# Optimization experiments

Hardware: AMD Instinct MI355X
Metric: run time of the kernel (lower is better)

The kernel has to match this reference:

```python
import jax, jax.numpy as jnp
import numpy as np

E, C, K, S = 8, 128, 512, 512  # embedding_dim, channels, kernel_size, stride
NEG_SLOPE = 0.01  # torch F.leaky_relu default


def setup_inputs() -> dict:
    key = jax.random.key(0)
    ks = jax.random.split(key, 11)
    B, T = 4, 1_000_000
    sc = 0.05
    return {
        "x": jax.random.normal(ks[0], (B, T, E), jnp.float32),
        # ctx_conv: Conv1d(E, 2C, K, stride=S) -> weight (2C, E, K), bias (2C,)
        "ctx_conv_w": jax.random.normal(ks[1], (2 * C, E, K), jnp.float32) * sc,
        "ctx_conv_b": jax.random.normal(ks[2], (2 * C,), jnp.float32) * sc,
        # ctx_share: Conv1d(C, C, 1) -> (C, C) pointwise
        "ctx_share_w": jax.random.normal(ks[3], (C, C), jnp.float32) * sc,
        "ctx_share_b": jax.random.normal(ks[4], (C,), jnp.float32) * sc,
        "main_conv_w": jax.random.normal(ks[5], (2 * C, E, K), jnp.float32) * sc,
        "main_conv_b": jax.random.normal(ks[6], (2 * C,), jnp.float32) * sc,
        "main_share_w": jax.random.normal(ks[7], (C, C), jnp.float32) * sc,
        "main_share_b": jax.random.normal(ks[8], (C,), jnp.float32) * sc,
        # gct_proj: Linear(C, C) -> weight (C, C) (y = g @ W.T + b)
        "gct_proj_w": jax.random.normal(ks[9], (C, C), jnp.float32) * sc,
        "gct_proj_b": jax.random.normal(ks[10], (C,), jnp.float32) * sc,
    }


def _leaky(x):
    return jnp.where(x >= 0, x, NEG_SLOPE * x)


def _glu(x):  # GLU over channel dim 1
    a, b = jnp.split(x, 2, axis=1)
    return a * jax.nn.sigmoid(b)


def _conv(z, w, b):
    # z: (B, Cin, T), w: (Cout, Cin, K) -> (B, Cout, T_out), stride S, VALID
    y = jax.lax.conv_general_dilated(z, w, (S,), 'VALID',
                                     dimension_numbers=('NCH', 'OIH', 'NCH'))
    return y + b[None, :, None]


def _branch_act(z, wc, bc, ws, bs):
    # glu(conv(z)) -> leaky_relu(1x1 share conv)
    h = _glu(_conv(z, wc, bc))                                   # (B, C, T_out)
    h = _leaky(jnp.einsum('oc,bct->bot', ws, h) + bs[None, :, None])
    return h


def reference(x, ctx_conv_w, ctx_conv_b, ctx_share_w, ctx_share_b,
              main_conv_w, main_conv_b, main_share_w, main_share_b,
              gct_proj_w, gct_proj_b):
    z = jnp.transpose(x, (0, 2, 1))  # (B, E, T)
    # Context branch: global max over time of ctx activations (GCG context).
    g = _branch_act(z, ctx_conv_w, ctx_conv_b, ctx_share_w, ctx_share_b)
    gct = jnp.max(g, axis=-1)  # (B, C)
    # Main branch with global channel gating.
    h = _branch_act(z, main_conv_w, main_conv_b, main_share_w, main_share_b)  # (B, C, T_out)
    q = jnp.tanh(gct @ gct_proj_w.T + gct_proj_b)                # (B, C)
    gate = jax.nn.sigmoid(jnp.einsum('bct,bc->bt', h, q))        # (B, T_out)
    out = jnp.max(h * gate[:, None, :], axis=-1)                 # (B, C)
    return out
```

## Files before the change

kernel.cpp:

```cpp
#include <hip/hip_runtime.h>
#include <hip/hip_bf16.h>
#include <cmath>

#define B_    4
#define T_    1000000
#define E_    8
#define C_    128
#define NCH   512
#define KK    4096
#define TOUT  1953
#define TP    1956
#define TPAD  2048
#define NT2   31

typedef __attribute__((ext_vector_type(8))) short bf16x8;
typedef __attribute__((ext_vector_type(4))) float f32x4;

__device__ __forceinline__ float sigmoidf_(float v) { return 1.f / (1.f + __expf(-v)); }

__device__ __forceinline__ void gload_lds16(const __hip_bfloat16* g, __hip_bfloat16* l) {
  __builtin_amdgcn_global_load_lds(
      (const __attribute__((address_space(1))) void*)(const void*)g,
      (__attribute__((address_space(3))) void*)(void*)l, 16, 0, 0);
}

__global__ __launch_bounds__(256) void prep_inputs(
    const float* __restrict__ x,
    const float* __restrict__ wc, const float* __restrict__ bc,
    const float* __restrict__ wm, const float* __restrict__ bm,
    __hip_bfloat16* __restrict__ xb2, __hip_bfloat16* __restrict__ Wn2,
    float* __restrict__ bias_t) {
  __shared__ float row[KK];
  const int bid = blockIdx.x;
  if (bid < NCH) {
    const int n = bid, br = n >> 8, o = n & 255;
    const float* wsrc = (br ? wm : wc) + (size_t)o * KK;
    for (int i = threadIdx.x; i < KK; i += 256) row[i] = wsrc[i];
    __syncthreads();
    const int nt = n >> 4, nr = n & 15;
    for (int k = threadIdx.x; k < KK; k += 256) {
      int kpos = k >> 3, e = k & 7;
      size_t addr = (((size_t)nt * 128 + (k >> 5)) * 64
                     + (size_t)((k >> 3) & 3) * 16 + nr) * 8 + (k & 7);
      Wn2[addr] = __float2bfloat16(row[e * 512 + kpos]);
    }
    if (threadIdx.x == 0) bias_t[n] = (br ? bm : bc)[o];
  } else {
    size_t gid = (size_t)(bid - NCH) * 256 + threadIdx.x;
    size_t idx8 = gid * 8;
    size_t b = idx8 >> 23, rem = idx8 & ((1ull << 23) - 1);
    int lane = (int)((rem >> 3) & 63);
    int kc   = (int)((rem >> 9) & 127);
    int tt   = (int)(rem >> 16);
    int t = tt * 16 + (lane & 15);
    int k = kc * 32 + (lane >> 4) * 8;
    union { __hip_bfloat16 h[8]; uint4 u; } o;
    if (t < TOUT) {
      const float* src = x + b * 8000000ull + (size_t)t * KK + k;
      float4 f0 = *(const float4*)(src);
      float4 f1 = *(const float4*)(src + 4);
      o.h[0] = __float2bfloat16(f0.x); o.h[1] = __float2bfloat16(f0.y);
      o.h[2] = __float2bfloat16(f0.z); o.h[3] = __float2bfloat16(f0.w);
      o.h[4] = __float2bfloat16(f1.x); o.h[5] = __float2bfloat16(f1.y);
      o.h[6] = __float2bfloat16(f1.z); o.h[7] = __float2bfloat16(f1.w);
    } else {
      o.u = make_uint4(0, 0, 0, 0);
    }
    *(uint4*)(xb2 + idx8) = o.u;
  }
}

__global__ __launch_bounds__(512, 2) void mfma_gemm(
    const __hip_bfloat16* __restrict__ xb2, const __hip_bfloat16* __restrict__ Wn2,
    float* __restrict__ u2) {
  __shared__ __hip_bfloat16 lds[2][16384];

  const int tid  = threadIdx.x;
  const int lane = tid & 63, wave = tid >> 6;
  const int wt = wave & 3, wn = wave >> 2;

  const int L   = blockIdx.x;
  const int xcd = L & 7;
  const int r   = L >> 3;
  const int nb  = r & 3;
  const int sh  = r >> 2;
  const int s   = sh * 8 + xcd;
  const int tblk = s & 15, b = s >> 4;
  const int t0 = tblk * 128, n0 = nb * 128;

  const size_t FR = 512;

  const __hip_bfloat16* gsrc[4];
  int cslot[4];
#pragma unroll
  for (int s2 = 0; s2 < 4; ++s2) {
    int c = wave * 4 + s2;
    cslot[c & 3] = c;
    if (c < 16) {
      gsrc[s2] = xb2 + ((size_t)(b * 128 + tblk * 8 + (c >> 1)) * 128 + (c & 1)) * FR
                 + (size_t)lane * 8;
    } else {
      gsrc[s2] = Wn2 + ((size_t)(nb * 8 + ((c - 16) >> 1)) * 128 + (c & 1)) * FR
                 + (size_t)lane * 8;
    }
  }

  f32x4 acc[2][4];
#pragma unroll
  for (int i = 0; i < 2; ++i)
#pragma unroll
    for (int j = 0; j < 4; ++j) acc[i][j] = (f32x4)(0.0f);

  auto STAGE = [&](int buf, int step) {
#pragma unroll
    for (int s2 = 0; s2 < 4; ++s2) {
      gload_lds16(gsrc[s2] + (size_t)step * 1024, &lds[buf][(size_t)cslot[s2] * FR]);
    }
  };

  auto COMPUTE = [&](int buf) {
    bf16x8 aF[2][2], bF[4][2];
#pragma unroll
    for (int i = 0; i < 2; ++i)
#pragma unroll
      for (int c = 0; c < 2; ++c)
        aF[i][c] = *(const bf16x8*)(&lds[buf][(size_t)((wt * 2 + i) * 2 + c) * FR
                                              + (size_t)lane * 8]);
#pragma unroll
    for (int j = 0; j < 4; ++j)
#pragma unroll
      for (int c = 0; c < 2; ++c)
        bF[j][c] = *(const bf16x8*)(&lds[buf][(size_t)(16 + (wn * 4 + j) * 2 + c) * FR
                                              + (size_t)lane * 8]);
#pragma unroll
    for (int c = 0; c < 2; ++c)
#pragma unroll
      for (int i = 0; i < 2; ++i)
#pragma unroll
        for (int j = 0; j < 4; ++j)
          acc[i][j] = __builtin_amdgcn_mfma_f32_16x16x32_bf16(aF[i][c], bF[j][c],
                                                              acc[i][j], 0, 0, 0);
  };

  STAGE(0, 0);
  __syncthreads();

  int cur = 0;
#pragma unroll 1
  for (int step = 0; step < 64; ++step) {
    if (step + 1 < 64) STAGE(cur ^ 1, step + 1);
    COMPUTE(cur);
    __syncthreads();
    cur ^= 1;
  }

  const int crow = (lane >> 4) * 4;
  const int ccol = lane & 15;
#pragma unroll
  for (int j = 0; j < 4; ++j) {
    int n = n0 + wn * 64 + j * 16 + ccol;
    float* urow = u2 + ((size_t)n * B_ + b) * TP;
#pragma unroll
    for (int i = 0; i < 2; ++i) {
      int t = t0 + wt * 32 + i * 16 + crow;
      if (t < TOUT) *(f32x4*)(urow + t) = acc[i][j];
    }
  }
}

__global__ __launch_bounds__(256) void share_act(
    const float* __restrict__ u2, const float* __restrict__ bias_t,
    const float* __restrict__ wsc, const float* __restrict__ bsc,
    const float* __restrict__ wsm, const float* __restrict__ bsm,
    float* __restrict__ hmain, float* __restrict__ gct_part) {
  __shared__ float Wl[128 * 132];
  __shared__ float ul[128 * 68];
  const int tid  = threadIdx.x;
  const int tile = blockIdx.x;
  const int b    = blockIdx.y;
  const int br   = blockIdx.z;
  const int t0   = tile * 64;
  const float* ws = br ? wsm : wsc;
  const float* bs = br ? bsm : bsc;

  for (int g = tid; g < 16384; g += 256) {
    int co = g >> 7, cp = g & 127;
    Wl[cp * 132 + co] = ws[g];
  }
  const size_t base_v = ((size_t)(br * 256) * B_ + b) * TP;
  const size_t base_g = ((size_t)(br * 256 + 128) * B_ + b) * TP;
  for (int g = tid; g < 8192; g += 256) {
    int cp = g >> 6, t = g & 63;
    float v = 0.f;
    if (t0 + t < TOUT) {
      float va = u2[base_v + (size_t)cp * B_ * TP + t0 + t] + bias_t[br * 256 + cp];
      float vg = u2[base_g + (size_t)cp * B_ * TP + t0 + t] + bias_t[br * 256 + 128 + cp];
      v = va * sigmoidf_(vg);
    }
    ul[cp * 68 + t] = v;
  }
  __syncthreads();

  const int ty = tid >> 4, tx = tid & 15;
  float acc[8][4];
#pragma unroll
  for (int i = 0; i < 8; ++i)
#pragma unroll
    for (int j = 0; j < 4; ++j) acc[i][j] = 0.f;

  for (int cp = 0; cp < 128; ++cp) {
    float4 a0 = *(const float4*)&Wl[cp*132 + ty*4];
    float4 a1 = *(const float4*)&Wl[cp*132 + 64 + ty*4];
    float4 b4 = *(const float4*)&ul[cp*68 + tx*4];
    float av[8] = {a0.x,a0.y,a0.z,a0.w,a1.x,a1.y,a1.z,a1.w};
    float bv[4] = {b4.x,b4.y,b4.z,b4.w};
#pragma unroll
    for (int i = 0; i < 8; ++i)
#pragma unroll
      for (int j = 0; j < 4; ++j) acc[i][j] = fmaf(av[i], bv[j], acc[i][j]);
  }

  float mloc[8];
#pragma unroll
  for (int i = 0; i < 8; ++i) mloc[i] = -INFINITY;
#pragma unroll
  for (int i = 0; i < 8; ++i) {
    int c = (i < 4) ? (ty*4 + i) : (64 + ty*4 + (i - 4));
    float bias = bs[c];
#pragma unroll
    for (int j = 0; j < 4; ++j) {
      int t = t0 + tx*4 + j;
      if (t >= TOUT) continue;
      float v = acc[i][j] + bias;
      v = (v >= 0.f) ? v : 0.01f * v;
      if (br == 1) {
        hmain[((size_t)b * 128 + c) * TOUT + t] = v;
      } else {
        mloc[i] = fmaxf(mloc[i], v);
      }
    }
  }
  if (br == 0) {
    __syncthreads();
    float* red = ul;
#pragma unroll
    for (int i = 0; i < 8; ++i) {
      int c = (i < 4) ? (ty*4 + i) : (64 + ty*4 + (i - 4));
      red[c * 16 + tx] = mloc[i];
    }
    __syncthreads();
    if (tid < 128) {
      float m = -INFINITY;
#pragma unroll
      for (int k = 0; k < 16; ++k) m = fmaxf(m, red[tid * 16 + k]);
      gct_part[((size_t)b * 128 + tid) * NT2 + tile] = m;
    }
  }
}

__global__ void gct_q(const float* __restrict__ gct_part, const float* __restrict__ wp,
                      const float* __restrict__ bp, float* __restrict__ q) {
  int b = blockIdx.x, tid = threadIdx.x;
  __shared__ float g[128];
  float m = -INFINITY;
  for (int tl = 0; tl < NT2; ++tl) m = fmaxf(m, gct_part[((size_t)b * 128 + tid) * NT2 + tl]);
  g[tid] = m;
  __syncthreads();
  float s = bp[tid];
  for (int c = 0; c < 128; ++c) s = fmaf(g[c], wp[tid * 128 + c], s);
  q[b * 128 + tid] = tanhf(s);
}

__global__ __launch_bounds__(256) void gate_max(
    const float* __restrict__ hmain, const float* __restrict__ q,
    float* __restrict__ out_part) {
  __shared__ float hl[128 * 68];
  __shared__ float ql[128];
  __shared__ float red[256];
  __shared__ float gl[64];
  int tid = threadIdx.x, tile = blockIdx.x, b = blockIdx.y;
  int t0 = tile * 64;
  for (int g = tid; g < 8192; g += 256) {
    int c = g >> 6, t = g & 63;
    hl[c * 68 + t] = (t0 + t < TOUT) ? hmain[((size_t)b * 128 + c) * TOUT + t0 + t] : 0.f;
  }
  if (tid < 128) ql[tid] = q[b * 128 + tid];
  __syncthreads();
  {
    int t = tid & 63, cy = tid >> 6;
    float s = 0.f;
#pragma unroll
    for (int cc = 0; cc < 32; ++cc) s = fmaf(hl[(cy * 32 + cc) * 68 + t], ql[cy * 32 + cc], s);
    red[cy * 64 + t] = s;
  }
  __syncthreads();
  if (tid < 64) {
    float s = red[tid] + red[64 + tid] + red[128 + tid] + red[192 + tid];
    gl[tid] = sigmoidf_(s);
  }
  __syncthreads();
  {
    int c = tid >> 1, th = tid & 1;
    float m = -INFINITY;
#pragma unroll
    for (int tt = 0; tt < 32; ++tt) {
      int t = th * 32 + tt;
      if (t0 + t < TOUT) m = fmaxf(m, hl[c * 68 + t] * gl[t]);
    }
    red[c * 2 + th] = m;
  }
  __syncthreads();
  if (tid < 128) out_part[((size_t)b * 128 + tid) * NT2 + tile] = fmaxf(red[tid * 2], red[tid * 2 + 1]);
}

__global__ void final_max(const float* __restrict__ out_part, float* __restrict__ out) {
  int idx = blockIdx.x * 256 + threadIdx.x;
  if (idx < 512) {
    float m = -INFINITY;
    for (int tl = 0; tl < NT2; ++tl) m = fmaxf(m, out_part[(size_t)idx * NT2 + tl]);
    out[idx] = m;
  }
}

extern "C" void kernel_launch(void* const* d_in, const int* in_sizes, int n_in,
                              void* d_out, int out_size, void* d_ws, size_t ws_size,
                              hipStream_t stream) {
  const float* x      = (const float*)d_in[0];
  const float* ctx_w  = (const float*)d_in[1];
  const float* ctx_b  = (const float*)d_in[2];
  const float* ctx_sw = (const float*)d_in[3];
  const float* ctx_sb = (const float*)d_in[4];
  const float* main_w = (const float*)d_in[5];
  const float* main_b = (const float*)d_in[6];
  const float* main_sw= (const float*)d_in[7];
  const float* main_sb= (const float*)d_in[8];
  const float* gp_w   = (const float*)d_in[9];
  const float* gp_b   = (const float*)d_in[10];

  char* w = (char*)d_ws;
  __hip_bfloat16* xb2 = (__hip_bfloat16*)(w);
  __hip_bfloat16* Wn2 = (__hip_bfloat16*)(w + 67108864);
  float* bias_t  = (float*)(w + 71303168);
  float* u2      = (float*)(w + 71305216);
  float* hmain   = (float*)(w + 87328768);
  float* gct_part= (float*)(w + 91328512);
  float* q       = (float*)(w + 91392000);
  float* out_part= (float*)(w + 91394048);

  prep_inputs<<<NCH + 16384, 256, 0, stream>>>(x, ctx_w, ctx_b, main_w, main_b,
                                               xb2, Wn2, bias_t);
  mfma_gemm<<<256, 512, 0, stream>>>(xb2, Wn2, u2);
  share_act<<<dim3(NT2, B_, 2), 256, 0, stream>>>(u2, bias_t, ctx_sw, ctx_sb,
                                                  main_sw, main_sb, hmain, gct_part);
  gct_q<<<B_, 128, 0, stream>>>(gct_part, gp_w, gp_b, q);
  gate_max<<<dim3(NT2, B_), 256, 0, stream>>>(hmain, q, out_part);
  final_max<<<2, 256, 0, stream>>>(out_part, (float*)d_out);
}
```

Measured before the change: 309.4 us.

## Fuse x fp32-to-bf16 conversion into GEMM A-tile loading

Drops the separate pass that converts x to a bf16 tiled buffer. The GEMM now loads fp32 x directly into registers, converts it to bf16, and writes it to LDS, software-pipelined against the MFMA compute of the current buffer, while B still uses direct global-to-LDS loads. This avoids writing and rereading a 64MB intermediate and shrinks the workspace. In exchange, register pressure rises and the A path now goes through VGPRs, with possibly less-coalesced strided fp32 reads.

Measured after the change: 351.4 us. 13.6% more time.

```diff
diff --git a/kernel.cpp b/kernel.cpp
--- a/kernel.cpp
+++ b/kernel.cpp
@@ -10,7 +10,6 @@
 #define KK    4096
 #define TOUT  1953
 #define TP    1956
-#define TPAD  2048
 #define NT2   31
 
 typedef __attribute__((ext_vector_type(8))) short bf16x8;
@@ -25,55 +24,29 @@
 }
 
 __global__ __launch_bounds__(256) void prep_inputs(
-    const float* __restrict__ x,
     const float* __restrict__ wc, const float* __restrict__ bc,
     const float* __restrict__ wm, const float* __restrict__ bm,
-    __hip_bfloat16* __restrict__ xb2, __hip_bfloat16* __restrict__ Wn2,
-    float* __restrict__ bias_t) {
+    __hip_bfloat16* __restrict__ Wn2, float* __restrict__ bias_t) {
   __shared__ float row[KK];
-  const int bid = blockIdx.x;
-  if (bid < NCH) {
-    const int n = bid, br = n >> 8, o = n & 255;
-    const float* wsrc = (br ? wm : wc) + (size_t)o * KK;
-    for (int i = threadIdx.x; i < KK; i += 256) row[i] = wsrc[i];
-    __syncthreads();
-    const int nt = n >> 4, nr = n & 15;
-    for (int k = threadIdx.x; k < KK; k += 256) {
-      int kpos = k >> 3, e = k & 7;
-      size_t addr = (((size_t)nt * 128 + (k >> 5)) * 64
-                     + (size_t)((k >> 3) & 3) * 16 + nr) * 8 + (k & 7);
-      Wn2[addr] = __float2bfloat16(row[e * 512 + kpos]);
-    }
-    if (threadIdx.x == 0) bias_t[n] = (br ? bm : bc)[o];
-  } else {
-    size_t gid = (size_t)(bid - NCH) * 256 + threadIdx.x;
-    size_t idx8 = gid * 8;
-    size_t b = idx8 >> 23, rem = idx8 & ((1ull << 23) - 1);
-    int lane = (int)((rem >> 3) & 63);
-    int kc   = (int)((rem >> 9) & 127);
-    int tt   = (int)(rem >> 16);
-    int t = tt * 16 + (lane & 15);
-    int k = kc * 32 + (lane >> 4) * 8;
-    union { __hip_bfloat16 h[8]; uint4 u; } o;
-    if (t < TOUT) {
-      const float* src = x + b * 8000000ull + (size_t)t * KK + k;
-      float4 f0 = *(const float4*)(src);
-      float4 f1 = *(const float4*)(src + 4);
-      o.h[0] = __float2bfloat16(f0.x); o.h[1] = __float2bfloat16(f0.y);
-      o.h[2] = __float2bfloat16(f0.z); o.h[3] = __float2bfloat16(f0.w);
-      o.h[4] = __float2bfloat16(f1.x); o.h[5] = __float2bfloat16(f1.y);
-      o.h[6] = __float2bfloat16(f1.z); o.h[7] = __float2bfloat16(f1.w);
-    } else {
-      o.u = make_uint4(0, 0, 0, 0);
-    }
-    *(uint4*)(xb2 + idx8) = o.u;
-  }
+  const int n = blockIdx.x, br = n >> 8, o = n & 255;
+  const float* wsrc = (br ? wm : wc) + (size_t)o * KK;
+  for (int i = threadIdx.x; i < KK; i += 256) row[i] = wsrc[i];
+  __syncthreads();
+  const int nt = n >> 4, nr = n & 15;
+  for (int k = threadIdx.x; k < KK; k += 256) {
+    int kpos = k >> 3, e = k & 7;
+    size_t addr = (((size_t)nt * 128 + (k >> 5)) * 64
+                   + (size_t)((k >> 3) & 3) * 16 + nr) * 8 + (k & 7);
+    Wn2[addr] = __float2bfloat16(row[e * 512 + kpos]);
+  }
+  if (threadIdx.x == 0) bias_t[n] = (br ? bm : bc)[o];
 }
 
 __global__ __launch_bounds__(512, 2) void mfma_gemm(
-    const __hip_bfloat16* __restrict__ xb2, const __hip_bfloat16* __restrict__ Wn2,
+    const float* __restrict__ x, const __hip_bfloat16* __restrict__ Wn2,
     float* __restrict__ u2) {
-  __shared__ __hip_bfloat16 lds[2][16384];
+  __shared__ __hip_bfloat16 As[2][8192];
+  __shared__ __hip_bfloat16 Bs[2][8192];
 
   const int tid  = threadIdx.x;
   const int lane = tid & 63, wave = tid >> 6;
@@ -88,22 +61,16 @@
   const int tblk = s & 15, b = s >> 4;
   const int t0 = tblk * 128, n0 = nb * 128;
 
-  const size_t FR = 512;
-
-  const __hip_bfloat16* gsrc[4];
-  int cslot[4];
-#pragma unroll
-  for (int s2 = 0; s2 < 4; ++s2) {
-    int c = wave * 4 + s2;
-    cslot[c & 3] = c;
-    if (c < 16) {
-      gsrc[s2] = xb2 + ((size_t)(b * 128 + tblk * 8 + (c >> 1)) * 128 + (c & 1)) * FR
-                 + (size_t)lane * 8;
-    } else {
-      gsrc[s2] = Wn2 + ((size_t)(nb * 8 + ((c - 16) >> 1)) * 128 + (c & 1)) * FR
-                 + (size_t)lane * 8;
-    }
-  }
+  int tA0 = t0 + (wave >> 1) * 16 + (lane & 15);
+  int tA1 = t0 + ((wave >> 1) + 4) * 16 + (lane & 15);
+  if (tA0 >= TOUT) tA0 = 0;
+  if (tA1 >= TOUT) tA1 = 0;
+  const int kAoff = (wave & 1) * 32 + (lane >> 4) * 8;
+  const float* pA0 = x + (size_t)b * 8000000ull + (size_t)tA0 * KK + kAoff;
+  const float* pA1 = x + (size_t)b * 8000000ull + (size_t)tA1 * KK + kAoff;
+
+  const __hip_bfloat16* gB0 = Wn2 + ((size_t)(nb * 8 + wave) * 128 + 0) * 512 + (size_t)lane * 8;
+  const __hip_bfloat16* gB1 = gB0 + 512;
 
   f32x4 acc[2][4];
 #pragma unroll
@@ -111,27 +78,47 @@
 #pragma unroll
     for (int j = 0; j < 4; ++j) acc[i][j] = (f32x4)(0.0f);
 
-  auto STAGE = [&](int buf, int step) {
-#pragma unroll
-    for (int s2 = 0; s2 < 4; ++s2) {
-      gload_lds16(gsrc[s2] + (size_t)step * 1024, &lds[buf][(size_t)cslot[s2] * FR]);
-    }
+  float4 ar00, ar01, ar10, ar11;
+
+  auto ALOAD = [&](int step) {
+    const float* p0 = pA0 + step * 64;
+    const float* p1 = pA1 + step * 64;
+    ar00 = *(const float4*)(p0);
+    ar01 = *(const float4*)(p0 + 4);
+    ar10 = *(const float4*)(p1);
+    ar11 = *(const float4*)(p1 + 4);
   };
-
+  auto BSTAGE = [&](int buf, int step) {
+    gload_lds16(gB0 + (size_t)step * 1024, &Bs[buf][(size_t)(wave * 2) * 512]);
+    gload_lds16(gB1 + (size_t)step * 1024, &Bs[buf][(size_t)(wave * 2 + 1) * 512]);
+  };
+  auto AWRITE = [&](int buf) {
+    union { __hip_bfloat16 h[8]; bf16x8 v; } u0, u1;
+    u0.h[0] = __float2bfloat16(ar00.x); u0.h[1] = __float2bfloat16(ar00.y);
+    u0.h[2] = __float2bfloat16(ar00.z); u0.h[3] = __float2bfloat16(ar00.w);
+    u0.h[4] = __float2bfloat16(ar01.x); u0.h[5] = __float2bfloat16(ar01.y);
+    u0.h[6] = __float2bfloat16(ar01.z); u0.h[7] = __float2bfloat16(ar01.w);
+    u1.h[0] = __float2bfloat16(ar10.x); u1.h[1] = __float2bfloat16(ar10.y);
+    u1.h[2] = __float2bfloat16(ar10.z); u1.h[3] = __float2bfloat16(ar10.w);
+    u1.h[4] = __float2bfloat16(ar11.x); u1.h[5] = __float2bfloat16(ar11.y);
+    u1.h[6] = __float2bfloat16(ar11.z); u1.h[7] = __float2bfloat16(ar11.w);
+    *(bf16x8*)&As[buf][(size_t)wave * 512 + (size_t)lane * 8] = u0.v;
+    *(bf16x8*)&As[buf][(size_t)(wave + 8) * 512 + (size_t)lane * 8] = u1.v;
+  };
   auto COMPUTE = [&](int buf) {
     bf16x8 aF[2][2], bF[4][2];
 #pragma unroll
     for (int i = 0; i < 2; ++i)
 #pragma unroll
       for (int c = 0; c < 2; ++c)
-        aF[i][c] = *(const bf16x8*)(&lds[buf][(size_t)((wt * 2 + i) * 2 + c) * FR
-                                              + (size_t)lane * 8]);
+        aF[i][c] = *(const bf16x8*)(&As[buf][(size_t)((wt * 2 + i) * 2 + c) * 512
+                                             + (size_t)lane * 8]);
 #pragma unroll
     for (int j = 0; j < 4; ++j)
 #pragma unroll
       for (int c = 0; c < 2; ++c)
-        bF[j][c] = *(const bf16x8*)(&lds[buf][(size_t)(16 + (wn * 4 + j) * 2 + c) * FR
-                                              + (size_t)lane * 8]);
+        bF[j][c] = *(const bf16x8*)(&Bs[buf][(size_t)((wn * 4 + j) * 2 + c) * 512
+                                             + (size_t)lane * 8]);
 #pragma unroll
     for (int c = 0; c < 2; ++c)
 #pragma unroll
@@ -142,14 +129,20 @@
                                                               acc[i][j], 0, 0, 0);
   };
 
-  STAGE(0, 0);
+  ALOAD(0);
+  BSTAGE(0, 0);
+  AWRITE(0);
   __syncthreads();
 
   int cur = 0;
 #pragma unroll 1
   for (int step = 0; step < 64; ++step) {
-    if (step + 1 < 64) STAGE(cur ^ 1, step + 1);
+    if (step + 1 < 64) {
+      ALOAD(step + 1);
+      BSTAGE(cur ^ 1, step + 1);
+    }
     COMPUTE(cur);
+    if (step + 1 < 64) AWRITE(cur ^ 1);
     __syncthreads();
     cur ^= 1;
   }
@@ -338,18 +331,16 @@
   const float* gp_b   = (const float*)d_in[10];
 
   char* w = (char*)d_ws;
-  __hip_bfloat16* xb2 = (__hip_bfloat16*)(w);
-  __hip_bfloat16* Wn2 = (__hip_bfloat16*)(w + 67108864);
-  float* bias_t  = (float*)(w + 71303168);
-  float* u2      = (float*)(w + 71305216);
-  float* hmain   = (float*)(w + 87328768);
-  float* gct_part= (float*)(w + 91328512);
-  float* q       = (float*)(w + 91392000);
-  float* out_part= (float*)(w + 91394048);
-
-  prep_inputs<<<NCH + 16384, 256, 0, stream>>>(x, ctx_w, ctx_b, main_w, main_b,
-                                               xb2, Wn2, bias_t);
-  mfma_gemm<<<256, 512, 0, stream>>>(xb2, Wn2, u2);
+  __hip_bfloat16* Wn2 = (__hip_bfloat16*)(w);
+  float* bias_t  = (float*)(w + 4194304);
+  float* u2      = (float*)(w + 4196352);
+  float* hmain   = (float*)(w + 20219904);
+  float* gct_part= (float*)(w + 24219648);
+  float* q       = (float*)(w + 24283136);
+  float* out_part= (float*)(w + 24285184);
+
+  prep_inputs<<<NCH, 256, 0, stream>>>(ctx_w, ctx_b, main_w, main_b, Wn2, bias_t);
+  mfma_gemm<<<256, 512, 0, stream>>>(x, Wn2, u2);
   share_act<<<dim3(NT2, B_, 2), 256, 0, stream>>>(u2, bias_t, ctx_sw, ctx_sb,
                                                   main_sw, main_sb, hmain, gct_part);
   gct_q<<<B_, 128, 0, stream>>>(gct_part, gp_w, gp_b, q);
```
